# Kernel optimization log

Measured on AMD Instinct MI355X. Metric: run time of the kernel, lower is better.

## Reference

```python
import jax, jax.numpy as jnp
import numpy as np

BATCH = 8
NUM_PRIORS = 57744
NUM_CLASSES = 81  # 80 fg classes + background (non-focal path: num_classes + 1)
NUM_OBJS = 20
POS_THRESHOLD = 0.5
NEG_THRESHOLD = 0.4
VARIANCES = (0.1, 0.2)
NEG_POS_RATIO = 3
LOSS_ALPHA_BBOX = 1.0
LOSS_ALPHA_CONF = 1.0


def setup_inputs() -> dict:
    key = jax.random.key(0)
    k1, k2, k3, k4, k5, k6, k7 = jax.random.split(key, 7)
    loc_data = jax.random.normal(k1, (BATCH, NUM_PRIORS, 4), dtype=jnp.float32)
    conf_data = jax.random.normal(k2, (BATCH, NUM_PRIORS, NUM_CLASSES), dtype=jnp.float32)
    # priors in center form (cx, cy, w, h), normalized coords
    cxcy = jax.random.uniform(k3, (NUM_PRIORS, 2), minval=0.0, maxval=1.0)
    wh = jax.random.uniform(k4, (NUM_PRIORS, 2), minval=0.02, maxval=0.3)
    priors = jnp.concatenate([cxcy, wh], axis=1).astype(jnp.float32)
    # gt boxes in point form (x1, y1, x2, y2)
    xy1 = jax.random.uniform(k5, (BATCH, NUM_OBJS, 2), minval=0.0, maxval=0.7)
    gwh = jax.random.uniform(k6, (BATCH, NUM_OBJS, 2), minval=0.05, maxval=0.3)
    gt_boxes = jnp.concatenate([xy1, xy1 + gwh], axis=-1).astype(jnp.float32)
    gt_labels = jax.random.randint(k7, (BATCH, NUM_OBJS), 1, NUM_CLASSES, dtype=jnp.int32)
    return {"loc_data": loc_data, "conf_data": conf_data, "priors": priors,
            "gt_boxes": gt_boxes, "gt_labels": gt_labels}


def point_form(p):  # (cx,cy,w,h) -> (x1,y1,x2,y2)
    return jnp.concatenate([p[:, :2] - p[:, 2:] / 2, p[:, :2] + p[:, 2:] / 2], axis=1)


def jaccard(a, b):  # a:[N,4] xyxy, b:[P,4] xyxy -> [N,P]
    lt = jnp.maximum(a[:, None, :2], b[None, :, :2])
    rb = jnp.minimum(a[:, None, 2:], b[None, :, 2:])
    wh = jnp.clip(rb - lt, 0.0, None)
    inter = wh[..., 0] * wh[..., 1]
    area_a = ((a[:, 2] - a[:, 0]) * (a[:, 3] - a[:, 1]))[:, None]
    area_b = ((b[:, 2] - b[:, 0]) * (b[:, 3] - b[:, 1]))[None, :]
    return inter / (area_a + area_b - inter)


def encode(matched, priors):  # matched xyxy [P,4], priors cxcywh [P,4]
    g_cxcy = (matched[:, :2] + matched[:, 2:]) / 2 - priors[:, :2]
    g_cxcy = g_cxcy / (VARIANCES[0] * priors[:, 2:])
    g_wh = jnp.log((matched[:, 2:] - matched[:, :2]) / priors[:, 2:]) / VARIANCES[1]
    return jnp.concatenate([g_cxcy, g_wh], axis=1)


def match_one(truths, labels, priors):
    # truths:[N,4] xyxy, labels:[N] int, priors:[P,4] cxcywh
    overlaps = jaccard(truths, point_form(priors))  # [N,P]
    best_truth_overlap = overlaps.max(axis=0)       # [P]
    best_truth_idx = overlaps.argmax(axis=0)        # [P]
    best_prior_idx = overlaps.argmax(axis=1)        # [N]
    # force-match each gt to its best prior
    best_truth_overlap = best_truth_overlap.at[best_prior_idx].set(2.0)
    best_truth_idx = best_truth_idx.at[best_prior_idx].set(jnp.arange(truths.shape[0]))
    matched = truths[best_truth_idx]                # [P,4]
    conf = labels[best_truth_idx].astype(jnp.int32)
    conf = jnp.where(best_truth_overlap < POS_THRESHOLD, -1, conf)  # ignore band
    conf = jnp.where(best_truth_overlap < NEG_THRESHOLD, 0, conf)   # background
    loc = encode(matched, priors)
    return loc, conf


def multibox_loss(loc_data, conf_data, priors, gt_boxes, gt_labels):
    loc_t, conf_t = jax.vmap(match_one, in_axes=(0, 0, None))(gt_boxes, gt_labels, priors)
    loc_t = jax.lax.stop_gradient(loc_t)  # Variable(requires_grad=False)
    pos = conf_t > 0                      # [B,P]
    num_pos = pos.sum()

    # localization: smooth-L1 over positives, mean per matched box
    diff = loc_data - loc_t
    ad = jnp.abs(diff)
    sl1 = jnp.where(ad < 1.0, 0.5 * diff * diff, ad - 0.5).sum(-1)  # [B,P]
    loss_B = LOSS_ALPHA_BBOX * (sl1 * pos).sum() / jnp.maximum(num_pos, 1)

    # hard negative mining on flattened batch (ratio 3, most-confident fg score)
    C = conf_data.shape[-1]
    conf_flat = conf_data.reshape(-1, C)
    ct = conf_t.reshape(-1)
    neg_cand = ct == 0
    score = conf_flat[:, 1:].max(axis=-1)
    score = jnp.where(neg_cand, score, -jnp.inf)
    order = jnp.argsort(-score)
    rank = jnp.zeros_like(order).at[order].set(jnp.arange(order.shape[0]))
    neg = (rank < NEG_POS_RATIO * num_pos) & neg_cand
    keep = (ct > 0) | neg

    logp = jax.nn.log_softmax(conf_flat, axis=-1)
    ce = -jnp.take_along_axis(logp, jnp.clip(ct, 0, C - 1)[:, None], axis=1)[:, 0]
    loss_C = LOSS_ALPHA_CONF * (ce * keep).sum() / jnp.maximum(keep.sum(), 1)

    return jnp.stack([loss_B, loss_C])  # [2]: (loss 'B', loss 'C')


def reference(loc_data, conf_data, priors, gt_boxes, gt_labels):
    return multibox_loss(loc_data, conf_data, priors, gt_boxes, gt_labels)
```

## Files before the change

### kernel.cpp

```cpp
#include <hip/hip_runtime.h>
#include <math.h>

#define BB 8
#define PP 57744
#define NOBJ 20
#define CC 81
#define ROWS (BB*PP)
#define CONFBLK ((ROWS + 255) / 256)
#define BPSPLIT 8
#define BPCHUNK (PP / BPSPLIT)
#define SELBLK 128

#define W_CNT  0
#define W_HA   64
#define W_HB   (W_HA + 8*2048)
#define W_HC   (W_HB + 8*2048)
#define W_ZERO (W_HC + 8*1024)
#define W_BP   W_ZERO
#define W_CONF (W_BP + 2560)
#define W_KEY  (W_CONF + ROWS)
#define W_CE   (W_KEY + ROWS)

#define SCOPE_AGENT __HIP_MEMORY_SCOPE_AGENT
#define VMEM_DRAIN() asm volatile("s_waitcnt vmcnt(0) lgkmcnt(0)" ::: "memory")

__device__ __forceinline__ unsigned keymap(float f) {
    unsigned u = __float_as_uint(f);
    return (u & 0x80000000u) ? ~u : (u | 0x80000000u);
}

__device__ __forceinline__ float smooth_l1(float d) {
    float a = fabsf(d);
    return a < 1.f ? 0.5f * d * d : a - 0.5f;
}

__device__ __forceinline__ unsigned aload_u(const unsigned* p) {
    return __hip_atomic_load(p, __ATOMIC_RELAXED, SCOPE_AGENT);
}
__device__ __forceinline__ int aload_i(const int* p) {
    return __hip_atomic_load(p, __ATOMIC_RELAXED, SCOPE_AGENT);
}
__device__ __forceinline__ float aload_f(const float* p) {
    return __hip_atomic_load(p, __ATOMIC_RELAXED, SCOPE_AGENT);
}
__device__ __forceinline__ void astore_i(int* p, int v) {
    __hip_atomic_store(p, v, __ATOMIC_RELAXED, SCOPE_AGENT);
}

template <int NB, bool ATOMIC>
__device__ int scan_bins(const unsigned* __restrict__ h, unsigned Kr,
                         unsigned* rem_out) {
    constexpr int BPT = NB / 256;
    __shared__ unsigned stot[256];
    __shared__ int sbin;
    __shared__ unsigned srem;
    __syncthreads();
    int i = threadIdx.x;
    unsigned v[BPT];
    unsigned tot = 0;
    #pragma unroll
    for (int j = 0; j < BPT; j++) {
        unsigned s = 0;
        #pragma unroll
        for (int c = 0; c < 8; c++) {
            const unsigned* p = h + c * NB + i * BPT + j;
            s += ATOMIC ? aload_u(p) : *p;
        }
        v[j] = s; tot += s;
    }
    if (i == 0) sbin = -1;
    stot[i] = tot; __syncthreads();
    for (int off = 1; off < 256; off <<= 1) {
        unsigned add = (i + off < 256) ? stot[i + off] : 0u;
        __syncthreads(); stot[i] += add; __syncthreads();
    }
    unsigned cum = (i < 255) ? stot[i + 1] : 0u;
    #pragma unroll
    for (int j = BPT - 1; j >= 0; j--) {
        unsigned nxt = cum;
        cum += v[j];
        if (cum >= Kr && nxt < Kr) { sbin = i * BPT + j; srem = Kr - nxt; }
    }
    __syncthreads();
    *rem_out = (sbin >= 0) ? srem : 0u;
    return sbin;
}

__global__ void k_best_prior(const float* __restrict__ priors,
                             const float* __restrict__ gt,
                             unsigned long long* __restrict__ bp8,
                             int* __restrict__ ws) {
    int n = blockIdx.x, b = blockIdx.y, z = blockIdx.z;
    int bid = n + NOBJ * (b + BB * z);
    int gz = bid * 256 + threadIdx.x;
    if (gz < W_ZERO) ws[gz] = 0;

    int p0 = z * BPCHUNK;
    int p1 = p0 + BPCHUNK;
    const float* t = gt + (b * NOBJ + n) * 4;
    float tx1 = t[0], ty1 = t[1], tx2 = t[2], ty2 = t[3];
    float ta = (tx2 - tx1) * (ty2 - ty1);
    unsigned long long best = 0ull;
    for (int p = p0 + threadIdx.x; p < p1; p += 256) {
        float4 pr = ((const float4*)priors)[p];
        float px1 = pr.x - pr.z * 0.5f, py1 = pr.y - pr.w * 0.5f;
        float px2 = pr.x + pr.z * 0.5f, py2 = pr.y + pr.w * 0.5f;
        float iw = fmaxf(fminf(tx2, px2) - fmaxf(tx1, px1), 0.f);
        float ih = fmaxf(fminf(ty2, py2) - fmaxf(ty1, py1), 0.f);
        float inter = iw * ih;
        float iou = inter / (ta + (px2 - px1) * (py2 - py1) - inter);
        unsigned long long pk = ((unsigned long long)__float_as_uint(iou) << 32)
                              | (unsigned long long)(0xFFFFFFFFu - (unsigned)p);
        if (pk > best) best = pk;
    }
    __shared__ unsigned long long sb[256];
    int tid = threadIdx.x;
    sb[tid] = best; __syncthreads();
    for (int s = 128; s > 0; s >>= 1) {
        if (tid < s && sb[tid + s] > sb[tid]) sb[tid] = sb[tid + s];
        __syncthreads();
    }
    if (tid == 0) bp8[(b * NOBJ + n) * BPSPLIT + z] = sb[0];
}

__global__ void k_match(const float* __restrict__ loc_data,
                        const float* __restrict__ priors,
                        const float* __restrict__ gt,
                        const int* __restrict__ labels,
                        const unsigned long long* __restrict__ bp8,
                        int* __restrict__ conf_t,
                        float* __restrict__ cnt_f,
                        int* __restrict__ cnt_i) {
    int b = blockIdx.y;
    int tid = threadIdx.x;
    int p = blockIdx.x * 256 + tid;
    __shared__ float st[NOBJ][4];
    __shared__ int slab[NOBJ], sbp[NOBJ];
    if (tid < NOBJ * 4) ((float*)st)[tid] = gt[b * NOBJ * 4 + tid];
    if (tid < NOBJ) {
        slab[tid] = labels[b * NOBJ + tid];
        unsigned long long m = 0ull;
        #pragma unroll
        for (int z = 0; z < BPSPLIT; z++) {
            unsigned long long v = bp8[(b * NOBJ + tid) * BPSPLIT + z];
            if (v > m) m = v;
        }
        sbp[tid] = (int)(0xFFFFFFFFu - (unsigned)m);
    }
    __syncthreads();
    float s_l1 = 0.f; int is_pos = 0;
    if (p < PP) {
        float4 pr = ((const float4*)priors)[p];
        float px1 = pr.x - pr.z * 0.5f, py1 = pr.y - pr.w * 0.5f;
        float px2 = pr.x + pr.z * 0.5f, py2 = pr.y + pr.w * 0.5f;
        float pa = (px2 - px1) * (py2 - py1);
        float best = -1.f; int bn = 0;
        for (int n = 0; n < NOBJ; n++) {
            float tx1 = st[n][0], ty1 = st[n][1], tx2 = st[n][2], ty2 = st[n][3];
            float iw = fmaxf(fminf(tx2, px2) - fmaxf(tx1, px1), 0.f);
            float ih = fmaxf(fminf(ty2, py2) - fmaxf(ty1, py1), 0.f);
            float inter = iw * ih;
            float iou = inter / ((tx2 - tx1) * (ty2 - ty1) + pa - inter);
            if (iou > best) { best = iou; bn = n; }
        }
        float ov = best;
        for (int n = 0; n < NOBJ; n++)
            if (sbp[n] == p) { bn = n; ov = 2.0f; }
        int conf = slab[bn];
        if (ov < 0.5f) conf = -1;
        if (ov < 0.4f) conf = 0;
        conf_t[b * PP + p] = conf;
        if (conf > 0) {
            is_pos = 1;
            float mx1 = st[bn][0], my1 = st[bn][1], mx2 = st[bn][2], my2 = st[bn][3];
            float gcx = ((mx1 + mx2) * 0.5f - pr.x) / (0.1f * pr.z);
            float gcy = ((my1 + my2) * 0.5f - pr.y) / (0.1f * pr.w);
            float gw = logf((mx2 - mx1) / pr.z) / 0.2f;
            float gh = logf((my2 - my1) / pr.w) / 0.2f;
            float4 ld = ((const float4*)loc_data)[b * PP + p];
            s_l1 = smooth_l1(ld.x - gcx) + smooth_l1(ld.y - gcy) +
                   smooth_l1(ld.z - gw) + smooth_l1(ld.w - gh);
        }
    }
    __shared__ float rs[256]; __shared__ int rc[256];
    rs[tid] = s_l1; rc[tid] = is_pos; __syncthreads();
    for (int s = 128; s > 0; s >>= 1) {
        if (tid < s) { rs[tid] += rs[tid + s]; rc[tid] += rc[tid + s]; }
        __syncthreads();
    }
    if (tid == 0) {
        if (rs[0] != 0.f) atomicAdd(&cnt_f[1], rs[0]);
        if (rc[0])        atomicAdd(&cnt_i[0], rc[0]);
    }
}

__global__ void __launch_bounds__(256) k_conf(const float* __restrict__ conf_data,
                                              const int* __restrict__ conf_t,
                                              unsigned* __restrict__ key,
                                              float* __restrict__ ce,
                                              float* __restrict__ cnt_f,
                                              unsigned* __restrict__ hA) {
    __shared__ unsigned lhist[2048];
    int tid = threadIdx.x;
    for (int j = tid; j < 2048; j += 256) lhist[j] = 0;
    __syncthreads();

    int row = blockIdx.x * 256 + tid;
    bool act = row < ROWS;
    int rr = act ? row : ROWS - 1;
    const float* x = conf_data + (size_t)rr * CC;
    int ct = conf_t[rr];

    float4 v[20];
    #pragma unroll
    for (int j = 0; j < 20; j++) __builtin_memcpy(&v[j], x + 4 * j, 16);
    float x80 = x[80];

    float f0 = v[0].y, f1 = v[0].z, f2 = v[0].w, f3 = x80;
    #pragma unroll
    for (int j = 1; j < 20; j++) {
        f0 = fmaxf(f0, v[j].x);
        f1 = fmaxf(f1, v[j].y);
        f2 = fmaxf(f2, v[j].z);
        f3 = fmaxf(f3, v[j].w);
    }
    float fg = fmaxf(fmaxf(f0, f1), fmaxf(f2, f3));
    float m = fmaxf(fg, v[0].x);

    const float LOG2E = 1.4426950408889634f;
    float e0 = 0.f, e1 = 0.f, e2 = 0.f, e3 = 0.f;
    #pragma unroll
    for (int j = 0; j < 20; j++) {
        e0 += exp2f((v[j].x - m) * LOG2E);
        e1 += exp2f((v[j].y - m) * LOG2E);
        e2 += exp2f((v[j].z - m) * LOG2E);
        e3 += exp2f((v[j].w - m) * LOG2E);
    }
    float e = (e0 + e1) + (e2 + e3) + exp2f((x80 - m) * LOG2E);

    float lse = m + log2f(e) * 0.6931471805599453f;
    int ctc = min(max(ct, 0), CC - 1);
    float xc = x[ctc];
    float cev = lse - xc;
    if (act) {
        ce[row] = cev;
        unsigned kv = (ct == 0) ? keymap(fg) : 0u;
        key[row] = kv;
        if (ct > 0) atomicAdd(&cnt_f[2], cev);
        if (ct == 0) atomicAdd(&lhist[kv >> 21], 1u);
    }
    __syncthreads();
    unsigned* hmy = hA + (blockIdx.x & 7) * 2048;
    for (int j = tid; j < 2048; j += 256)
        if (lhist[j]) atomicAdd(&hmy[j], lhist[j]);
}

__global__ void __launch_bounds__(256) k_sel(const unsigned* __restrict__ key,
                                             const float* __restrict__ ce,
                                             int* __restrict__ cnt_i,
                                             float* __restrict__ cnt_f,
                                             const unsigned* __restrict__ hA,
                                             unsigned* __restrict__ hB,
                                             unsigned* __restrict__ hC,
                                             float* __restrict__ out) {
    __shared__ unsigned lh[2048];
    __shared__ int amLast;
    int tid = threadIdx.x;
    const uint4* k4 = (const uint4*)key;
    int n4 = ROWS / 4;

    unsigned T = 0xFFFFFFFFu; int eqS = 0;
    unsigned Kr = 3u * (unsigned)cnt_i[0];
    bool decided = (Kr == 0);
    unsigned prefixA = 0, remB = 0;
    if (!decided) {
        int binA = scan_bins<2048, false>(hA, Kr, &remB);
        if (binA < 0) { T = 0u; eqS = 0; decided = true; }
        else prefixA = (unsigned)binA;
    }

    if (!decided) {
        for (int j = tid; j < 2048; j += 256) lh[j] = 0;
        __syncthreads();
        for (int r = blockIdx.x * 256 + tid; r < n4; r += gridDim.x * 256) {
            uint4 k = k4[r];
            if ((k.x >> 21) == prefixA) atomicAdd(&lh[(k.x >> 10) & 0x7FFu], 1u);
            if ((k.y >> 21) == prefixA) atomicAdd(&lh[(k.y >> 10) & 0x7FFu], 1u);
            if ((k.z >> 21) == prefixA) atomicAdd(&lh[(k.z >> 10) & 0x7FFu], 1u);
            if ((k.w >> 21) == prefixA) atomicAdd(&lh[(k.w >> 10) & 0x7FFu], 1u);
        }
        __syncthreads();
        {
            unsigned* hmy = hB + (blockIdx.x & 7) * 2048;
            for (int j = tid; j < 2048; j += 256)
                if (lh[j]) atomicAdd(&hmy[j], lh[j]);
        }
        VMEM_DRAIN();
        if (tid == 0)
            amLast = (__hip_atomic_fetch_add((unsigned*)&cnt_i[12], 1u,
                       __ATOMIC_RELAXED, SCOPE_AGENT) == (unsigned)(gridDim.x - 1));
        __syncthreads();
        if (amLast) {
            unsigned remC; int binB = scan_bins<2048, true>(hB, remB, &remC);
            if (binB < 0) { binB = 0; remC = 0; }
            if (tid == 0) {
                astore_i(&cnt_i[15], (int)((prefixA << 11) | (unsigned)binB));
                astore_i(&cnt_i[16], (int)remC);
                VMEM_DRAIN();
                astore_i(&cnt_i[14], 1);
            }
        }
        if (tid == 0) {
            while (aload_i(&cnt_i[14]) == 0) __builtin_amdgcn_s_sleep(8);
        }
        __syncthreads();
        unsigned prefixAB = (unsigned)aload_i(&cnt_i[15]);
        unsigned KrC = (unsigned)aload_i(&cnt_i[16]);

        for (int j = tid; j < 1024; j += 256) lh[j] = 0;
        __syncthreads();
        for (int r = blockIdx.x * 256 + tid; r < n4; r += gridDim.x * 256) {
            uint4 k = k4[r];
            if ((k.x >> 10) == prefixAB) atomicAdd(&lh[k.x & 0x3FFu], 1u);
            if ((k.y >> 10) == prefixAB) atomicAdd(&lh[k.y & 0x3FFu], 1u);
            if ((k.z >> 10) == prefixAB) atomicAdd(&lh[k.z & 0x3FFu], 1u);
            if ((k.w >> 10) == prefixAB) atomicAdd(&lh[k.w & 0x3FFu], 1u);
        }
        __syncthreads();
        {
            unsigned* hmy = hC + (blockIdx.x & 7) * 1024;
            for (int j = tid; j < 1024; j += 256)
                if (lh[j]) atomicAdd(&hmy[j], lh[j]);
        }
        VMEM_DRAIN();
        if (tid == 0)
            amLast = (__hip_atomic_fetch_add((unsigned*)&cnt_i[17], 1u,
                       __ATOMIC_RELAXED, SCOPE_AGENT) == (unsigned)(gridDim.x - 1));
        __syncthreads();
        if (amLast) {
            unsigned remD; int binC = scan_bins<1024, true>(hC, KrC, &remD);
            if (binC < 0) { binC = 0; remD = 0; }
            if (tid == 0) {
                astore_i(&cnt_i[10], (int)((prefixAB << 10) | (unsigned)binC));
                astore_i(&cnt_i[11], (int)remD);
                VMEM_DRAIN();
                astore_i(&cnt_i[21], 1);
            }
        }
        if (tid == 0) {
            while (aload_i(&cnt_i[21]) == 0) __builtin_amdgcn_s_sleep(8);
        }
        __syncthreads();
        T = (unsigned)aload_i(&cnt_i[10]);
        eqS = aload_i(&cnt_i[11]);
    }

    float s = 0.f; int c = 0;
    for (int r = blockIdx.x * 256 + tid; r < n4; r += gridDim.x * 256) {
        uint4 k = k4[r];
        #define DO_ONE(comp, idx) { \
            unsigned kk = k.comp; \
            if (kk) { \
                bool selr = false; \
                if (kk > T) selr = true; \
                else if (kk == T) { int slot = atomicAdd(&cnt_i[5], 1); selr = slot < eqS; } \
                if (selr) { s += ce[4 * r + idx]; c++; } \
            } }
        DO_ONE(x, 0) DO_ONE(y, 1) DO_ONE(z, 2) DO_ONE(w, 3)
        #undef DO_ONE
    }
    __shared__ float rs[256]; __shared__ int rc[256];
    rs[tid] = s; rc[tid] = c; __syncthreads();
    for (int st = 128; st > 0; st >>= 1) {
        if (tid < st) { rs[tid] += rs[tid + st]; rc[tid] += rc[tid + st]; }
        __syncthreads();
    }
    if (tid == 0) {
        if (rs[0] != 0.f) atomicAdd(&cnt_f[3], rs[0]);
        if (rc[0])        atomicAdd(&cnt_i[4], rc[0]);
    }
    VMEM_DRAIN();
    if (tid == 0 &&
        __hip_atomic_fetch_add((unsigned*)&cnt_i[13], 1u,
            __ATOMIC_RELAXED, SCOPE_AGENT) == (unsigned)(gridDim.x - 1)) {
        int np = aload_i(&cnt_i[0]);
        int nn = aload_i(&cnt_i[4]);
        float f1 = aload_f(&cnt_f[1]);
        float f2 = aload_f(&cnt_f[2]);
        float f3 = aload_f(&cnt_f[3]);
        out[0] = f1 / (float)max(np, 1);
        out[1] = (f2 + f3) / (float)max(np + nn, 1);
    }
}

extern "C" void kernel_launch(void* const* d_in, const int* in_sizes, int n_in,
                              void* d_out, int out_size, void* d_ws, size_t ws_size,
                              hipStream_t stream) {
    const float* loc    = (const float*)d_in[0];
    const float* conf   = (const float*)d_in[1];
    const float* priors = (const float*)d_in[2];
    const float* gt     = (const float*)d_in[3];
    const int*   labels = (const int*)d_in[4];
    float* out = (float*)d_out;
    int*      wi = (int*)d_ws;
    float*    wf = (float*)d_ws;
    unsigned* wu = (unsigned*)d_ws;
    unsigned long long* wbp = (unsigned long long*)(wi + W_BP);

    k_best_prior<<<dim3(NOBJ, BB, BPSPLIT), 256, 0, stream>>>(priors, gt, wbp, wi);
    k_match<<<dim3((PP + 255) / 256, BB), 256, 0, stream>>>(
        loc, priors, gt, labels, wbp, wi + W_CONF, wf, wi);
    k_conf<<<CONFBLK, 256, 0, stream>>>(conf, wi + W_CONF, wu + W_KEY,
                                        wf + W_CE, wf, wu + W_HA);
    k_sel<<<SELBLK, 256, 0, stream>>>(wu + W_KEY, wf + W_CE, wi, wf,
                                      wu + W_HA, wu + W_HB, wu + W_HC, out);
}
```

Before: 360.5 us.

## Fuse prior matching into confidence kernel and use wave-level positive reductions

Removes the separate matching kernel: each confidence-kernel thread now computes IoU matching for its own row, working out which batch its row belongs to, since a block can straddle two batches. This eliminates the conf_t round trip through global memory and one kernel launch. The per-positive global float atomics are replaced by wavefront shuffle reductions with one atomic per wave. The cost is extra registers and ALU work in the already register-heavy conf kernel, which may lower occupancy.

```diff
diff --git a/kernel.cpp b/kernel.cpp
--- a/kernel.cpp
+++ b/kernel.cpp
@@ -17,8 +17,7 @@
 #define W_HC   (W_HB + 8*2048)
 #define W_ZERO (W_HC + 8*1024)
 #define W_BP   W_ZERO
-#define W_CONF (W_BP + 2560)
-#define W_KEY  (W_CONF + ROWS)
+#define W_KEY  (W_BP + 2560)
 #define W_CE   (W_KEY + ROWS)
 
 #define SCOPE_AGENT __HIP_MEMORY_SCOPE_AGENT
@@ -123,98 +122,73 @@
     if (tid == 0) bp8[(b * NOBJ + n) * BPSPLIT + z] = sb[0];
 }
 
-__global__ void k_match(const float* __restrict__ loc_data,
-                        const float* __restrict__ priors,
-                        const float* __restrict__ gt,
-                        const int* __restrict__ labels,
-                        const unsigned long long* __restrict__ bp8,
-                        int* __restrict__ conf_t,
-                        float* __restrict__ cnt_f,
-                        int* __restrict__ cnt_i) {
-    int b = blockIdx.y;
+__global__ void __launch_bounds__(256) k_conf(const float* __restrict__ conf_data,
+                                              const float* __restrict__ loc_data,
+                                              const float* __restrict__ priors,
+                                              const float* __restrict__ gt,
+                                              const int* __restrict__ labels,
+                                              const unsigned long long* __restrict__ bp8,
+                                              unsigned* __restrict__ key,
+                                              float* __restrict__ ce,
+                                              float* __restrict__ cnt_f,
+                                              int* __restrict__ cnt_i,
+                                              unsigned* __restrict__ hA) {
+    __shared__ unsigned lhist[2048];
+    __shared__ float st2[2][NOBJ][4];
+    __shared__ int slab2[2][NOBJ], sbp2[2][NOBJ];
     int tid = threadIdx.x;
-    int p = blockIdx.x * 256 + tid;
-    __shared__ float st[NOBJ][4];
-    __shared__ int slab[NOBJ], sbp[NOBJ];
-    if (tid < NOBJ * 4) ((float*)st)[tid] = gt[b * NOBJ * 4 + tid];
-    if (tid < NOBJ) {
-        slab[tid] = labels[b * NOBJ + tid];
+    int row0 = blockIdx.x * 256;
+    int b0 = row0 / PP;
+
+    for (int j = tid; j < 2048; j += 256) lhist[j] = 0;
+    if (tid < 2 * NOBJ * 4 && b0 * NOBJ * 4 + tid < BB * NOBJ * 4)
+        ((float*)st2)[tid] = gt[b0 * NOBJ * 4 + tid];
+    if (tid < 2 * NOBJ && b0 * NOBJ + tid < BB * NOBJ) {
+        ((int*)slab2)[tid] = labels[b0 * NOBJ + tid];
         unsigned long long m = 0ull;
         #pragma unroll
         for (int z = 0; z < BPSPLIT; z++) {
-            unsigned long long v = bp8[(b * NOBJ + tid) * BPSPLIT + z];
+            unsigned long long v = bp8[(b0 * NOBJ + tid) * BPSPLIT + z];
             if (v > m) m = v;
         }
-        sbp[tid] = (int)(0xFFFFFFFFu - (unsigned)m);
+        ((int*)sbp2)[tid] = (int)(0xFFFFFFFFu - (unsigned)m);
     }
     __syncthreads();
-    float s_l1 = 0.f; int is_pos = 0;
-    if (p < PP) {
-        float4 pr = ((const float4*)priors)[p];
-        float px1 = pr.x - pr.z * 0.5f, py1 = pr.y - pr.w * 0.5f;
-        float px2 = pr.x + pr.z * 0.5f, py2 = pr.y + pr.w * 0.5f;
-        float pa = (px2 - px1) * (py2 - py1);
-        float best = -1.f; int bn = 0;
-        for (int n = 0; n < NOBJ; n++) {
-            float tx1 = st[n][0], ty1 = st[n][1], tx2 = st[n][2], ty2 = st[n][3];
-            float iw = fmaxf(fminf(tx2, px2) - fmaxf(tx1, px1), 0.f);
-            float ih = fmaxf(fminf(ty2, py2) - fmaxf(ty1, py1), 0.f);
-            float inter = iw * ih;
-            float iou = inter / ((tx2 - tx1) * (ty2 - ty1) + pa - inter);
-            if (iou > best) { best = iou; bn = n; }
-        }
-        float ov = best;
-        for (int n = 0; n < NOBJ; n++)
-            if (sbp[n] == p) { bn = n; ov = 2.0f; }
-        int conf = slab[bn];
-        if (ov < 0.5f) conf = -1;
-        if (ov < 0.4f) conf = 0;
-        conf_t[b * PP + p] = conf;
-        if (conf > 0) {
-            is_pos = 1;
-            float mx1 = st[bn][0], my1 = st[bn][1], mx2 = st[bn][2], my2 = st[bn][3];
-            float gcx = ((mx1 + mx2) * 0.5f - pr.x) / (0.1f * pr.z);
-            float gcy = ((my1 + my2) * 0.5f - pr.y) / (0.1f * pr.w);
-            float gw = logf((mx2 - mx1) / pr.z) / 0.2f;
-            float gh = logf((my2 - my1) / pr.w) / 0.2f;
-            float4 ld = ((const float4*)loc_data)[b * PP + p];
-            s_l1 = smooth_l1(ld.x - gcx) + smooth_l1(ld.y - gcy) +
-                   smooth_l1(ld.z - gw) + smooth_l1(ld.w - gh);
-        }
-    }
-    __shared__ float rs[256]; __shared__ int rc[256];
-    rs[tid] = s_l1; rc[tid] = is_pos; __syncthreads();
-    for (int s = 128; s > 0; s >>= 1) {
-        if (tid < s) { rs[tid] += rs[tid + s]; rc[tid] += rc[tid + s]; }
-        __syncthreads();
-    }
-    if (tid == 0) {
-        if (rs[0] != 0.f) atomicAdd(&cnt_f[1], rs[0]);
-        if (rc[0])        atomicAdd(&cnt_i[0], rc[0]);
-    }
-}
-
-__global__ void __launch_bounds__(256) k_conf(const float* __restrict__ conf_data,
-                                              const int* __restrict__ conf_t,
-                                              unsigned* __restrict__ key,
-                                              float* __restrict__ ce,
-                                              float* __restrict__ cnt_f,
-                                              unsigned* __restrict__ hA) {
-    __shared__ unsigned lhist[2048];
-    int tid = threadIdx.x;
-    for (int j = tid; j < 2048; j += 256) lhist[j] = 0;
-    __syncthreads();
-
-    int row = blockIdx.x * 256 + tid;
+
+    int row = row0 + tid;
     bool act = row < ROWS;
     int rr = act ? row : ROWS - 1;
     const float* x = conf_data + (size_t)rr * CC;
-    int ct = conf_t[rr];
 
     float4 v[20];
     #pragma unroll
     for (int j = 0; j < 20; j++) __builtin_memcpy(&v[j], x + 4 * j, 16);
     float x80 = x[80];
+
+    int bi = (rr >= (b0 + 1) * PP) ? 1 : 0;
+    int p = rr - (b0 + bi) * PP;
+    float4 pr = ((const float4*)priors)[p];
+    float px1 = pr.x - pr.z * 0.5f, py1 = pr.y - pr.w * 0.5f;
+    float px2 = pr.x + pr.z * 0.5f, py2 = pr.y + pr.w * 0.5f;
+    float pa = (px2 - px1) * (py2 - py1);
+    float best = -1.f; int bn = 0;
+    #pragma unroll
+    for (int n = 0; n < NOBJ; n++) {
+        float tx1 = st2[bi][n][0], ty1 = st2[bi][n][1];
+        float tx2 = st2[bi][n][2], ty2 = st2[bi][n][3];
+        float iw = fmaxf(fminf(tx2, px2) - fmaxf(tx1, px1), 0.f);
+        float ih = fmaxf(fminf(ty2, py2) - fmaxf(ty1, py1), 0.f);
+        float inter = iw * ih;
+        float iou = inter / ((tx2 - tx1) * (ty2 - ty1) + pa - inter);
+        if (iou > best) { best = iou; bn = n; }
+    }
+    float ov = best;
+    #pragma unroll
+    for (int n = 0; n < NOBJ; n++)
+        if (sbp2[bi][n] == p) { bn = n; ov = 2.0f; }
+    int ct = slab2[bi][bn];
+    if (ov < 0.5f) ct = -1;
+    if (ov < 0.4f) ct = 0;
 
     float f0 = v[0].y, f1 = v[0].z, f2 = v[0].w, f3 = x80;
     #pragma unroll
@@ -239,15 +213,42 @@
     float e = (e0 + e1) + (e2 + e3) + exp2f((x80 - m) * LOG2E);
 
     float lse = m + log2f(e) * 0.6931471805599453f;
-    int ctc = min(max(ct, 0), CC - 1);
-    float xc = x[ctc];
+    float xc = (ct > 0) ? x[ct] : v[0].x;
     float cev = lse - xc;
+
+    float s_l1 = 0.f;
+    bool pos = act && ct > 0;
+    if (pos) {
+        float mx1 = st2[bi][bn][0], my1 = st2[bi][bn][1];
+        float mx2 = st2[bi][bn][2], my2 = st2[bi][bn][3];
+        float gcx = ((mx1 + mx2) * 0.5f - pr.x) / (0.1f * pr.z);
+        float gcy = ((my1 + my2) * 0.5f - pr.y) / (0.1f * pr.w);
+        float gw = logf((mx2 - mx1) / pr.z) / 0.2f;
+        float gh = logf((my2 - my1) / pr.w) / 0.2f;
+        float4 ld = ((const float4*)loc_data)[rr];
+        s_l1 = smooth_l1(ld.x - gcx) + smooth_l1(ld.y - gcy) +
+               smooth_l1(ld.z - gw) + smooth_l1(ld.w - gh);
+    }
     if (act) {
         ce[row] = cev;
         unsigned kv = (ct == 0) ? keymap(fg) : 0u;
         key[row] = kv;
-        if (ct > 0) atomicAdd(&cnt_f[2], cev);
         if (ct == 0) atomicAdd(&lhist[kv >> 21], 1u);
+    }
+    unsigned long long bal = __ballot(pos);
+    if (bal) {
+        float sl = pos ? s_l1 : 0.f;
+        float pc = pos ? cev : 0.f;
+        #pragma unroll
+        for (int off = 32; off > 0; off >>= 1) {
+            sl += __shfl_xor(sl, off);
+            pc += __shfl_xor(pc, off);
+        }
+        if ((tid & 63) == 0) {
+            atomicAdd(&cnt_i[0], (int)__popcll(bal));
+            atomicAdd(&cnt_f[1], sl);
+            atomicAdd(&cnt_f[2], pc);
+        }
     }
     __syncthreads();
     unsigned* hmy = hA + (blockIdx.x & 7) * 2048;
@@ -408,10 +409,8 @@
     unsigned long long* wbp = (unsigned long long*)(wi + W_BP);
 
     k_best_prior<<<dim3(NOBJ, BB, BPSPLIT), 256, 0, stream>>>(priors, gt, wbp, wi);
-    k_match<<<dim3((PP + 255) / 256, BB), 256, 0, stream>>>(
-        loc, priors, gt, labels, wbp, wi + W_CONF, wf, wi);
-    k_conf<<<CONFBLK, 256, 0, stream>>>(conf, wi + W_CONF, wu + W_KEY,
-                                        wf + W_CE, wf, wu + W_HA);
+    k_conf<<<CONFBLK, 256, 0, stream>>>(conf, loc, priors, gt, labels, wbp,
+                                        wu + W_KEY, wf + W_CE, wf, wi, wu + W_HA);
     k_sel<<<SELBLK, 256, 0, stream>>>(wu + W_KEY, wf + W_CE, wi, wf,
                                       wu + W_HA, wu + W_HB, wu + W_HC, out);
 }
```

After: 465.4 us. 1.29x slower.
